# Optimization experiments

Hardware: AMD Instinct MI355X
Metric: run time of the kernel (lower is better)

## Reference

```python
import jax, jax.numpy as jnp
import numpy as np

# B trajectories, L spline knots, D data channels, H hidden, W MLP width, OUT outputs
B, L, D, H, W, OUT = 1024, 200, 32, 64, 128, 16
N_STEPS = 100  # dt0 = (ts[-1]-ts[0]) / 100 in the source -> fixed-step Heun over the span


def _mlp3(x, W1, b1, W2, b2, W3, b3, act, final_act=None):
    h = act(x @ W1.T + b1)
    h = act(h @ W2.T + b2)
    o = h @ W3.T + b3
    return final_act(o) if final_act is not None else o


def setup_inputs() -> dict:
    key = jax.random.key(0)
    ks = jax.random.split(key, 16)
    f32 = jnp.float32

    def rn(k, shape, scale):
        return jax.random.normal(k, shape, f32) * scale

    def lin(kk, out_d, in_d):
        kw, kb = jax.random.split(kk)
        s = 1.0 / float(np.sqrt(in_d))
        return rn(kw, (out_d, in_d), s), rn(kb, (out_d,), s)

    inp = {"ts": jnp.arange(L, dtype=f32)}
    for i, n in enumerate(["coef_d", "coef_c", "coef_b", "coef_a"]):
        inp[n] = rn(ks[i], (B, L - 1, D), 0.1)
    inp["iW1"], inp["ib1"] = lin(ks[4], W, D)
    inp["iW2"], inp["ib2"] = lin(ks[5], W, W)
    inp["iW3"], inp["ib3"] = lin(ks[6], H, W)
    inp["fW1"], inp["fb1"] = lin(ks[7], W, H)
    inp["fW2"], inp["fb2"] = lin(ks[8], W, W)
    inp["fW3"], inp["fb3"] = lin(ks[9], H * D, W)
    inp["dW1"], inp["db1"] = lin(ks[10], 128, H)
    inp["dW2"], inp["db2"] = lin(ks[11], 128, 128)
    inp["dW3"], inp["db3"] = lin(ks[12], OUT, 128)
    return inp


def reference(ts, coef_d, coef_c, coef_b, coef_a,
              iW1, ib1, iW2, ib2, iW3, ib3,
              fW1, fb1, fW2, fb2, fW3, fb3,
              dW1, db1, dW2, db2, dW3, db3):
    sp = jax.nn.softplus
    # X(t0) = a[:, 0] (cubic-spline eval at left knot has frac = 0)
    y0 = _mlp3(coef_a[:, 0], iW1, ib1, iW2, ib2, iW3, ib3, sp, final_act=sp)  # [B, H]
    t0 = ts[0]
    dt = (ts[-1] - t0) / N_STEPS

    def dXdt(t):  # cubic spline derivative at scalar time t -> [B, D]
        i = jnp.clip(jnp.searchsorted(ts, t, side="right") - 1, 0, L - 2)
        frac = t - ts[i]
        return coef_b[:, i] + frac * (2.0 * coef_c[:, i] + 3.0 * frac * coef_d[:, i])

    def vf(t, y):  # ControlTerm(func, control).to_ode(): f(y) @ dX/dt
        f = _mlp3(y, fW1, fb1, fW2, fb2, fW3, fb3, sp).reshape(B, H, D)
        return jnp.einsum("bhd,bd->bh", f, dXdt(t))

    def heun_step(y, k):
        t = t0 + k * dt
        k1 = vf(t, y)
        k2 = vf(t + dt, y + dt * k1)
        return y + 0.5 * dt * (k1 + k2), None

    yT, _ = jax.lax.scan(heun_step, y0, jnp.arange(N_STEPS, dtype=ts.dtype))
    # decoder: Linear->relu->Linear->relu->Linear
    return _mlp3(yT, dW1, db1, dW2, db2, dW3, db3, jax.nn.relu)  # [B, OUT]
```

## Files before the change

### kernel.cpp

```cpp
#include <hip/hip_runtime.h>

#define NT 512
#define TRAJ 4

constexpr int Lk = 200;
constexpr int NSTEPS = 100;

__device__ __forceinline__ float sp_act(float x) {
    return fmaxf(x, 0.0f) + log1pf(expf(-fabsf(x)));
}

__global__ void fw3_transpose(const float* __restrict__ w, float* __restrict__ wT) {
    int idx = blockIdx.x * 256 + threadIdx.x;
    int k = idx >> 11;
    int n = idx & 2047;
    wT[idx] = w[n * 128 + k];
}

template<int O, int I>
__device__ __forceinline__ void stage_T(const float* __restrict__ g, float* __restrict__ T) {
    for (int base = threadIdx.x * 4; base < O * I; base += NT * 4) {
        const float4 w = *(const float4*)(g + base);
        const int o = base / I;
        const int i = base % I;
        T[(i + 0) * O + o] = w.x;
        T[(i + 1) * O + o] = w.y;
        T[(i + 2) * O + o] = w.z;
        T[(i + 3) * O + o] = w.w;
    }
}

template<int I, int O, int ACT>
__device__ __forceinline__ void mlp_layer(const float* __restrict__ T,
                                          const float* __restrict__ bias,
                                          const float* __restrict__ in, int inStride,
                                          float* __restrict__ out, int outStride) {
    const int tid = threadIdx.x;
    constexpr int TOT = TRAJ * O;
    for (int e = tid; e < TOT; e += NT) {
        const int t = e / O;
        const int o = e % O;
        const float* inr = in + t * inStride;
        float acc = bias[o];
        #pragma unroll 4
        for (int i = 0; i < I; ++i) acc = fmaf(inr[i], T[i * O + o], acc);
        if (ACT == 1) acc = sp_act(acc);
        else if (ACT == 2) acc = fmaxf(acc, 0.0f);
        out[t * outStride + o] = acc;
    }
}

__device__ __forceinline__ void evalvf(float t,
                                       const float* __restrict__ yin,
                                       float* __restrict__ kout,
                                       const float* __restrict__ wT1,
                                       const float* __restrict__ wT2,
                                       const float* __restrict__ fb1s,
                                       const float* __restrict__ fb2s,
                                       float* __restrict__ h1s,
                                       float* __restrict__ h2s,
                                       float* __restrict__ dXs,
                                       const float* __restrict__ ts,
                                       const float* __restrict__ coef_b,
                                       const float* __restrict__ coef_c,
                                       const float* __restrict__ coef_d,
                                       int bbase,
                                       const float4* __restrict__ wp,
                                       float4 fb3r)
{
    const int tid = threadIdx.x;

    if (tid < TRAJ * 32) {
        int i = (int)floorf(t);
        i = min(max(i, 0), Lk - 2);
        const float frac = t - ts[i];
        const int tt = tid >> 5, d = tid & 31;
        const size_t off = ((size_t)(bbase + tt) * 199 + (size_t)i) * 32 + d;
        dXs[tid] = coef_b[off] + frac * (2.0f * coef_c[off] + 3.0f * frac * coef_d[off]);
    }
    mlp_layer<64, 128, 1>(wT1, fb1s, yin, 64, h1s, 128);
    __syncthreads();
    mlp_layer<128, 128, 1>(wT2, fb2s, h1s, 128, h2s, 128);
    __syncthreads();

    float4 acc[TRAJ];
    #pragma unroll
    for (int t4 = 0; t4 < TRAJ; ++t4) acc[t4] = make_float4(0.f, 0.f, 0.f, 0.f);

    for (int k0 = 0; k0 < 128; k0 += 4) {
        const float4 w0 = wp[(k0 + 0) * 512];
        const float4 w1 = wp[(k0 + 1) * 512];
        const float4 w2 = wp[(k0 + 2) * 512];
        const float4 w3 = wp[(k0 + 3) * 512];
        #pragma unroll
        for (int t4 = 0; t4 < TRAJ; ++t4) {
            const float4 h = *(const float4*)(h2s + t4 * 128 + k0);
            float4 a = acc[t4];
            a.x = fmaf(h.x, w0.x, a.x); a.y = fmaf(h.x, w0.y, a.y); a.z = fmaf(h.x, w0.z, a.z); a.w = fmaf(h.x, w0.w, a.w);
            a.x = fmaf(h.y, w1.x, a.x); a.y = fmaf(h.y, w1.y, a.y); a.z = fmaf(h.y, w1.z, a.z); a.w = fmaf(h.y, w1.w, a.w);
            a.x = fmaf(h.z, w2.x, a.x); a.y = fmaf(h.z, w2.y, a.y); a.z = fmaf(h.z, w2.z, a.z); a.w = fmaf(h.z, w2.w, a.w);
            a.x = fmaf(h.w, w3.x, a.x); a.y = fmaf(h.w, w3.y, a.y); a.z = fmaf(h.w, w3.z, a.z); a.w = fmaf(h.w, w3.w, a.w);
            acc[t4] = a;
        }
    }

    const int dbase = 4 * (tid & 7);
    float part[TRAJ];
    #pragma unroll
    for (int t4 = 0; t4 < TRAJ; ++t4) {
        const float4 dx = *(const float4*)(dXs + t4 * 32 + dbase);
        part[t4] = (acc[t4].x + fb3r.x) * dx.x + (acc[t4].y + fb3r.y) * dx.y +
                   (acc[t4].z + fb3r.z) * dx.z + (acc[t4].w + fb3r.w) * dx.w;
    }
    #pragma unroll
    for (int m = 1; m < 8; m <<= 1) {
        #pragma unroll
        for (int t4 = 0; t4 < TRAJ; ++t4) part[t4] += __shfl_xor(part[t4], m, 64);
    }
    if ((tid & 7) == 0) {
        const int h = tid >> 3;
        #pragma unroll
        for (int t4 = 0; t4 < TRAJ; ++t4) kout[t4 * 64 + h] = part[t4];
    }
    __syncthreads();
}

__global__ __launch_bounds__(NT, 1)
void cde_kernel(const float* __restrict__ ts,
                const float* __restrict__ coef_d, const float* __restrict__ coef_c,
                const float* __restrict__ coef_b, const float* __restrict__ coef_a,
                const float* __restrict__ iW1, const float* __restrict__ ib1,
                const float* __restrict__ iW2, const float* __restrict__ ib2,
                const float* __restrict__ iW3, const float* __restrict__ ib3,
                const float* __restrict__ fW1, const float* __restrict__ fb1,
                const float* __restrict__ fW2, const float* __restrict__ fb2,
                const float* __restrict__ fb3,
                const float* __restrict__ dW1, const float* __restrict__ db1,
                const float* __restrict__ dW2, const float* __restrict__ db2,
                const float* __restrict__ dW3, const float* __restrict__ db3,
                const float* __restrict__ fW3T,
                float* __restrict__ outp)
{
    __shared__ float wreg[28672];
    __shared__ float h1s[TRAJ * 128], h2s[TRAJ * 128];
    __shared__ float ys[TRAJ * 64], ys2[TRAJ * 64], k1s[TRAJ * 64], k2s[TRAJ * 64];
    __shared__ float dXs[TRAJ * 32], a0s[TRAJ * 32];
    __shared__ float fb1s[128], fb2s[128];

    const int tid = threadIdx.x;
    const int bbase = blockIdx.x * TRAJ;

    const float ts0 = ts[0];
    const float dt = (ts[Lk - 1] - ts0) / (float)NSTEPS;
    const float4 fb3r = *((const float4*)fb3 + tid);
    const float4* wp = (const float4*)fW3T + tid;

    if (tid < TRAJ * 32) {
        const int t = tid >> 5, d = tid & 31;
        a0s[t * 32 + d] = coef_a[((size_t)(bbase + t) * 199) * 32 + d];
    }
    stage_T<128, 32>(iW1, wreg);
    stage_T<128, 128>(iW2, wreg + 32 * 128);
    stage_T<64, 128>(iW3, wreg + 32 * 128 + 128 * 128);
    if (tid < 128) { fb1s[tid] = fb1[tid]; fb2s[tid] = fb2[tid]; }
    __syncthreads();
    mlp_layer<32, 128, 1>(wreg, ib1, a0s, 32, h1s, 128);
    __syncthreads();
    mlp_layer<128, 128, 1>(wreg + 32 * 128, ib2, h1s, 128, h2s, 128);
    __syncthreads();
    mlp_layer<128, 64, 1>(wreg + 32 * 128 + 128 * 128, ib3, h2s, 128, ys, 64);
    __syncthreads();

    stage_T<128, 64>(fW1, wreg);
    stage_T<128, 128>(fW2, wreg + 64 * 128);
    __syncthreads();

    for (int step = 0; step < NSTEPS; ++step) {
        const float t1 = ts0 + (float)step * dt;
        evalvf(t1, ys, k1s, wreg, wreg + 64 * 128, fb1s, fb2s, h1s, h2s, dXs,
               ts, coef_b, coef_c, coef_d, bbase, wp, fb3r);
        if (tid < TRAJ * 64) ys2[tid] = ys[tid] + dt * k1s[tid];
        __syncthreads();
        evalvf(t1 + dt, ys2, k2s, wreg, wreg + 64 * 128, fb1s, fb2s, h1s, h2s, dXs,
               ts, coef_b, coef_c, coef_d, bbase, wp, fb3r);
        if (tid < TRAJ * 64) ys[tid] += 0.5f * dt * (k1s[tid] + k2s[tid]);
        __syncthreads();
    }

    stage_T<128, 64>(dW1, wreg);
    stage_T<128, 128>(dW2, wreg + 64 * 128);
    stage_T<16, 128>(dW3, wreg + 64 * 128 + 128 * 128);
    __syncthreads();
    mlp_layer<64, 128, 2>(wreg, db1, ys, 64, h1s, 128);
    __syncthreads();
    mlp_layer<128, 128, 2>(wreg + 64 * 128, db2, h1s, 128, h2s, 128);
    __syncthreads();
    mlp_layer<128, 16, 0>(wreg + 64 * 128 + 128 * 128, db3, h2s, 128,
                          outp + (size_t)bbase * 16, 16);
}

extern "C" void kernel_launch(void* const* d_in, const int* in_sizes, int n_in,
                              void* d_out, int out_size, void* d_ws, size_t ws_size,
                              hipStream_t stream) {
    (void)in_sizes; (void)n_in; (void)out_size; (void)ws_size;
    const float* ts     = (const float*)d_in[0];
    const float* coef_d = (const float*)d_in[1];
    const float* coef_c = (const float*)d_in[2];
    const float* coef_b = (const float*)d_in[3];
    const float* coef_a = (const float*)d_in[4];
    const float* iW1 = (const float*)d_in[5];  const float* ib1 = (const float*)d_in[6];
    const float* iW2 = (const float*)d_in[7];  const float* ib2 = (const float*)d_in[8];
    const float* iW3 = (const float*)d_in[9];  const float* ib3 = (const float*)d_in[10];
    const float* fW1 = (const float*)d_in[11]; const float* fb1 = (const float*)d_in[12];
    const float* fW2 = (const float*)d_in[13]; const float* fb2 = (const float*)d_in[14];
    const float* fW3 = (const float*)d_in[15]; const float* fb3 = (const float*)d_in[16];
    const float* dW1 = (const float*)d_in[17]; const float* db1 = (const float*)d_in[18];
    const float* dW2 = (const float*)d_in[19]; const float* db2 = (const float*)d_in[20];
    const float* dW3 = (const float*)d_in[21]; const float* db3 = (const float*)d_in[22];

    float* fW3T = (float*)d_ws;

    fw3_transpose<<<1024, 256, 0, stream>>>(fW3, fW3T);
    cde_kernel<<<256, NT, 0, stream>>>(ts, coef_d, coef_c, coef_b, coef_a,
                                       iW1, ib1, iW2, ib2, iW3, ib3,
                                       fW1, fb1, fW2, fb2, fb3,
                                       dW1, db1, dW2, db2, dW3, db3,
                                       fW3T, (float*)d_out);
}
```

Measured before the change: 2.676 ms.

## Software-pipeline fW3 weight loads with nontemporal prefetch and raise occupancy hint

Issues the first batch of fW3 weight loads before the first two MLP layers so global-memory latency overlaps with that compute. It then double-buffers eight rows at a time inside the k-loop, using nontemporal loads and vector-type FMAs. Launch bounds change from 1 to 2 blocks per SM. The extra in-flight registers may conflict with the tighter register budget from the new launch bound, and with about 112KB of static shared memory two blocks may not fit per CU anyway.

```diff
diff --git a/kernel.cpp b/kernel.cpp
--- a/kernel.cpp
+++ b/kernel.cpp
@@ -5,6 +5,8 @@
 
 constexpr int Lk = 200;
 constexpr int NSTEPS = 100;
+
+typedef float f32x4 __attribute__((ext_vector_type(4)));
 
 __device__ __forceinline__ float sp_act(float x) {
     return fmaxf(x, 0.0f) + log1pf(expf(-fabsf(x)));
@@ -65,7 +67,7 @@
                                        const float* __restrict__ coef_c,
                                        const float* __restrict__ coef_d,
                                        int bbase,
-                                       const float4* __restrict__ wp,
+                                       const f32x4* __restrict__ wq,
                                        float4 fb3r)
 {
     const int tid = threadIdx.x;
@@ -78,28 +80,42 @@
         const size_t off = ((size_t)(bbase + tt) * 199 + (size_t)i) * 32 + d;
         dXs[tid] = coef_b[off] + frac * (2.0f * coef_c[off] + 3.0f * frac * coef_d[off]);
     }
+
+    f32x4 nw[8];
+    #pragma unroll
+    for (int j = 0; j < 8; ++j) nw[j] = __builtin_nontemporal_load(wq + j * 512);
+
     mlp_layer<64, 128, 1>(wT1, fb1s, yin, 64, h1s, 128);
     __syncthreads();
     mlp_layer<128, 128, 1>(wT2, fb2s, h1s, 128, h2s, 128);
     __syncthreads();
 
-    float4 acc[TRAJ];
-    #pragma unroll
-    for (int t4 = 0; t4 < TRAJ; ++t4) acc[t4] = make_float4(0.f, 0.f, 0.f, 0.f);
-
-    for (int k0 = 0; k0 < 128; k0 += 4) {
-        const float4 w0 = wp[(k0 + 0) * 512];
-        const float4 w1 = wp[(k0 + 1) * 512];
-        const float4 w2 = wp[(k0 + 2) * 512];
-        const float4 w3 = wp[(k0 + 3) * 512];
+    f32x4 acc[TRAJ];
+    #pragma unroll
+    for (int t4 = 0; t4 < TRAJ; ++t4) acc[t4] = (f32x4)0.0f;
+
+    for (int k0 = 0; k0 < 128; k0 += 8) {
+        f32x4 cw[8];
+        #pragma unroll
+        for (int j = 0; j < 8; ++j) cw[j] = nw[j];
+        if (k0 + 8 < 128) {
+            #pragma unroll
+            for (int j = 0; j < 8; ++j)
+                nw[j] = __builtin_nontemporal_load(wq + (k0 + 8 + j) * 512);
+        }
         #pragma unroll
         for (int t4 = 0; t4 < TRAJ; ++t4) {
-            const float4 h = *(const float4*)(h2s + t4 * 128 + k0);
-            float4 a = acc[t4];
-            a.x = fmaf(h.x, w0.x, a.x); a.y = fmaf(h.x, w0.y, a.y); a.z = fmaf(h.x, w0.z, a.z); a.w = fmaf(h.x, w0.w, a.w);
-            a.x = fmaf(h.y, w1.x, a.x); a.y = fmaf(h.y, w1.y, a.y); a.z = fmaf(h.y, w1.z, a.z); a.w = fmaf(h.y, w1.w, a.w);
-            a.x = fmaf(h.z, w2.x, a.x); a.y = fmaf(h.z, w2.y, a.y); a.z = fmaf(h.z, w2.z, a.z); a.w = fmaf(h.z, w2.w, a.w);
-            a.x = fmaf(h.w, w3.x, a.x); a.y = fmaf(h.w, w3.y, a.y); a.z = fmaf(h.w, w3.z, a.z); a.w = fmaf(h.w, w3.w, a.w);
+            const f32x4 hA = *(const f32x4*)(h2s + t4 * 128 + k0);
+            const f32x4 hB = *(const f32x4*)(h2s + t4 * 128 + k0 + 4);
+            f32x4 a = acc[t4];
+            a += hA.x * cw[0];
+            a += hA.y * cw[1];
+            a += hA.z * cw[2];
+            a += hA.w * cw[3];
+            a += hB.x * cw[4];
+            a += hB.y * cw[5];
+            a += hB.z * cw[6];
+            a += hB.w * cw[7];
             acc[t4] = a;
         }
     }
@@ -125,7 +141,7 @@
     __syncthreads();
 }
 
-__global__ __launch_bounds__(NT, 1)
+__global__ __launch_bounds__(NT, 2)
 void cde_kernel(const float* __restrict__ ts,
                 const float* __restrict__ coef_d, const float* __restrict__ coef_c,
                 const float* __restrict__ coef_b, const float* __restrict__ coef_a,
@@ -153,7 +169,7 @@
     const float ts0 = ts[0];
     const float dt = (ts[Lk - 1] - ts0) / (float)NSTEPS;
     const float4 fb3r = *((const float4*)fb3 + tid);
-    const float4* wp = (const float4*)fW3T + tid;
+    const f32x4* wq = (const f32x4*)fW3T + tid;
 
     if (tid < TRAJ * 32) {
         const int t = tid >> 5, d = tid & 31;
@@ -178,11 +194,11 @@
     for (int step = 0; step < NSTEPS; ++step) {
         const float t1 = ts0 + (float)step * dt;
         evalvf(t1, ys, k1s, wreg, wreg + 64 * 128, fb1s, fb2s, h1s, h2s, dXs,
-               ts, coef_b, coef_c, coef_d, bbase, wp, fb3r);
+               ts, coef_b, coef_c, coef_d, bbase, wq, fb3r);
         if (tid < TRAJ * 64) ys2[tid] = ys[tid] + dt * k1s[tid];
         __syncthreads();
         evalvf(t1 + dt, ys2, k2s, wreg, wreg + 64 * 128, fb1s, fb2s, h1s, h2s, dXs,
-               ts, coef_b, coef_c, coef_d, bbase, wp, fb3r);
+               ts, coef_b, coef_c, coef_d, bbase, wq, fb3r);
         if (tid < TRAJ * 64) ys[tid] += 0.5f * dt * (k1s[tid] + k2s[tid]);
         __syncthreads();
     }
```

Result: slower. 3.411 ms (+27.4%).
